# Kernel optimization log

Measured on AMD Instinct MI355X. Metric: run time of the kernel, lower is better.

## Reference

```python
import jax, jax.numpy as jnp
import numpy as np

N_NODES = 100000
N_EDGES = 1600000
F_IN = 128
DIM = 64
N_CLASSES = 40


def setup_inputs() -> dict:
    key = jax.random.key(0)
    ks = jax.random.split(key, 12)
    x = jax.random.normal(ks[0], (N_NODES, F_IN), dtype=jnp.float32)
    edge_index = jax.random.randint(ks[1], (2, N_EDGES), 0, N_NODES, dtype=jnp.int64)
    s = lambda fan_in: 1.0 / np.sqrt(fan_in)
    W1 = jax.random.uniform(ks[2], (F_IN, DIM), jnp.float32, -s(F_IN), s(F_IN))
    b1 = jax.random.uniform(ks[3], (DIM,), jnp.float32, -s(F_IN), s(F_IN))
    W2 = jax.random.uniform(ks[4], (DIM, DIM), jnp.float32, -s(DIM), s(DIM))
    b2 = jax.random.uniform(ks[5], (DIM,), jnp.float32, -s(DIM), s(DIM))
    Wf1 = jax.random.uniform(ks[6], (DIM, DIM), jnp.float32, -s(DIM), s(DIM))
    bf1 = jax.random.uniform(ks[7], (DIM,), jnp.float32, -s(DIM), s(DIM))
    Wf2 = jax.random.uniform(ks[8], (DIM, N_CLASSES), jnp.float32, -s(DIM), s(DIM))
    bf2 = jax.random.uniform(ks[9], (N_CLASSES,), jnp.float32, -s(DIM), s(DIM))
    return {"x": x, "edge_index": edge_index, "W1": W1, "b1": b1,
            "W2": W2, "b2": b2, "Wf1": Wf1, "bf1": bf1, "Wf2": Wf2, "bf2": bf2}


def _gin_agg(h, src, dst, n_nodes):
    # sum_{j in N(i)} h_j : gather along src, scatter-add to dst
    return jax.ops.segment_sum(h[src], dst, num_segments=n_nodes)


def reference(x, edge_index, W1, b1, W2, b2, Wf1, bf1, Wf2, bf2):
    src, dst = edge_index[0], edge_index[1]
    n = x.shape[0]
    # GINConv(Linear), eps=0: Linear(x + sum_neighbors)
    h = jax.nn.relu((x + _gin_agg(x, src, dst, n)) @ W1 + b1)
    h = jax.nn.relu((h + _gin_agg(h, src, dst, n)) @ W2 + b2)
    h = jax.nn.relu(h @ Wf1 + bf1)  # dropout p=0.5 is identity at inference
    logits = h @ Wf2 + bf2
    return jax.nn.log_softmax(logits, axis=1)
```

## Files before the change

kernel.cpp:

```cpp
#include <hip/hip_runtime.h>

#define NN 100000
#define NE 1600000
#define F_IN 128
#define DIM 64
#define NC 40
#define NB 196
#define MAXBE 10240

typedef unsigned short ushort_t;
typedef __attribute__((ext_vector_type(8))) short bf16x8;
typedef __attribute__((ext_vector_type(4))) float f32x4;

static __device__ __forceinline__ float b2f(ushort_t u) {
  return __uint_as_float(((unsigned)u) << 16);
}
static __device__ __forceinline__ ushort_t f2b(float f) {
  unsigned x = __float_as_uint(f);
  return (ushort_t)((x + 0x7fffu + ((x >> 16) & 1u)) >> 16);
}
static __device__ __forceinline__ unsigned pack2(float a, float b) {
  return (unsigned)f2b(a) | ((unsigned)f2b(b) << 16);
}

__global__ __launch_bounds__(256) void k_prep(const float* __restrict__ W1,
                                              const float* __restrict__ W2,
                                              const float* __restrict__ Wf1,
                                              const float* __restrict__ Wf2,
                                              ushort_t* __restrict__ W1T,
                                              ushort_t* __restrict__ W2T,
                                              ushort_t* __restrict__ Wf1T,
                                              ushort_t* __restrict__ Wf2T,
                                              int* __restrict__ bcur) {
  int t = threadIdx.x;
  if (t < NB) bcur[t] = 0;
  for (int i = t; i < 64 * 128; i += 256) { int c = i >> 7, k = i & 127; W1T[i] = f2b(W1[k * 64 + c]); }
  for (int i = t; i < 64 * 64; i += 256)  { int c = i >> 6, k = i & 63;  W2T[i] = f2b(W2[k * 64 + c]); }
  for (int i = t; i < 64 * 64; i += 256)  { int c = i >> 6, k = i & 63;  Wf1T[i] = f2b(Wf1[k * 64 + c]); }
  for (int i = t; i < 48 * 64; i += 256)  { int c = i >> 6, k = i & 63;  Wf2T[i] = (c < NC) ? f2b(Wf2[k * NC + c]) : (ushort_t)0; }
}

__global__ __launch_bounds__(256) void k_part(const int* __restrict__ src,
                                              const int* __restrict__ dst,
                                              int* __restrict__ bcur,
                                              unsigned* __restrict__ part) {
  __shared__ int hist[NB];
  __shared__ int gbase[NB];
  int t = threadIdx.x;
  for (int i = t; i < NB; i += 256) hist[i] = 0;
  __syncthreads();
  int e0 = blockIdx.x * 4096;
  int s[16], dd[16], r[16];
#pragma unroll
  for (int i = 0; i < 16; ++i) {
    int e = e0 + i * 256 + t;
    if (e < NE) {
      dd[i] = dst[e];
      s[i] = src[e];
      r[i] = atomicAdd(&hist[dd[i] >> 9], 1);
    }
  }
  __syncthreads();
  for (int i = t; i < NB; i += 256)
    gbase[i] = hist[i] ? atomicAdd(&bcur[i], hist[i]) : 0;
  __syncthreads();
#pragma unroll
  for (int i = 0; i < 16; ++i) {
    int e = e0 + i * 256 + t;
    if (e < NE) {
      int b = dd[i] >> 9;
      part[(size_t)b * MAXBE + gbase[b] + r[i]] = ((unsigned)(dd[i] & 511) << 17) | (unsigned)s[i];
    }
  }
}

__global__ __launch_bounds__(256) void k_csr(const int* __restrict__ bcur,
                                             const unsigned* __restrict__ part,
                                             int* __restrict__ cnt,
                                             int* __restrict__ offs,
                                             int* __restrict__ slots) {
  __shared__ unsigned pb[MAXBE];
  __shared__ ushort_t rk[MAXBE];
  __shared__ int lcnt[512], loff[512];
  int b = blockIdx.x, t = threadIdx.x;
  int start = b * MAXBE;
  int m = bcur[b];
  if (m > MAXBE) m = MAXBE;
  lcnt[t] = 0; lcnt[t + 256] = 0;
  __syncthreads();
  for (int i = t; i < m; i += 256) {
    unsigned v = part[start + i];
    pb[i] = v;
    rk[i] = (ushort_t)atomicAdd(&lcnt[v >> 17], 1);
  }
  __syncthreads();
  int o0 = lcnt[t], o1 = lcnt[t + 256];
  __syncthreads();
  for (int off = 1; off < 512; off <<= 1) {
    int v0 = (t >= off) ? lcnt[t - off] : 0;
    int v1 = (t + 256 >= off) ? lcnt[t + 256 - off] : 0;
    __syncthreads();
    lcnt[t] += v0;
    lcnt[t + 256] += v1;
    __syncthreads();
  }
  loff[t] = lcnt[t] - o0;
  loff[t + 256] = lcnt[t + 256] - o1;
  int node0 = b << 9;
  if (node0 + t < NN)       { cnt[node0 + t] = o0;       offs[node0 + t] = start + loff[t]; }
  if (node0 + t + 256 < NN) { cnt[node0 + t + 256] = o1; offs[node0 + t + 256] = start + loff[t + 256]; }
  __syncthreads();
  for (int i = t; i < m; i += 256) {
    unsigned v = pb[i];
    slots[start + loff[v >> 17] + rk[i]] = (int)(v & 0x1FFFFu);
  }
}

__global__ __launch_bounds__(256) void k_agg(const ushort_t* __restrict__ yb,
                                             const int* __restrict__ cnt,
                                             const int* __restrict__ offs,
                                             const int* __restrict__ slots,
                                             const float* __restrict__ bias,
                                             ushort_t* __restrict__ hb) {
  int wv = threadIdx.x >> 6, l = threadIdx.x & 63;
  int h = l >> 5;
  int n = blockIdx.x * 8 + wv * 2 + h;
  int li = l & 31;
  int g = (l >> 3) & 3;
  int q = l & 7;
  int cb = q * 16;
  int deg = cnt[n], start = offs[n];
  deg = deg > 64 ? 64 : deg;
  int sv0 = (li < deg) ? slots[start + li] : 0;
  int sv1 = (32 + li < deg) ? slots[start + 32 + li] : 0;
  int dego = __shfl_xor(deg, 32);
  int degmax = deg > dego ? deg : dego;
  float acc[8];
#pragma unroll
  for (int i = 0; i < 8; ++i) acc[i] = 0.f;
  const char* ybp = (const char*)yb;
  int hbase = h << 5;
  for (int j = 0; j < degmax; j += 16) {
    int i0 = j + g, i1 = j + 4 + g, i2 = j + 8 + g, i3 = j + 12 + g;
    int sa, sb, sc, sd;
    if (j < 32) {
      sa = __shfl(sv0, hbase + i0); sb = __shfl(sv0, hbase + i1);
      sc = __shfl(sv0, hbase + i2); sd = __shfl(sv0, hbase + i3);
    } else {
      sa = __shfl(sv1, hbase + (i0 & 31)); sb = __shfl(sv1, hbase + (i1 & 31));
      sc = __shfl(sv1, hbase + (i2 & 31)); sd = __shfl(sv1, hbase + (i3 & 31));
    }
    uint4 u0 = {0,0,0,0}, u1 = {0,0,0,0}, u2 = {0,0,0,0}, u3 = {0,0,0,0};
    if (i0 < deg) u0 = *(const uint4*)(ybp + (size_t)sa * 128 + cb);
    if (i1 < deg) u1 = *(const uint4*)(ybp + (size_t)sb * 128 + cb);
    if (i2 < deg) u2 = *(const uint4*)(ybp + (size_t)sc * 128 + cb);
    if (i3 < deg) u3 = *(const uint4*)(ybp + (size_t)sd * 128 + cb);
    acc[0] += __uint_as_float(u0.x << 16);  acc[1] += __uint_as_float(u0.x & 0xffff0000u);
    acc[2] += __uint_as_float(u0.y << 16);  acc[3] += __uint_as_float(u0.y & 0xffff0000u);
    acc[4] += __uint_as_float(u0.z << 16);  acc[5] += __uint_as_float(u0.z & 0xffff0000u);
    acc[6] += __uint_as_float(u0.w << 16);  acc[7] += __uint_as_float(u0.w & 0xffff0000u);
    acc[0] += __uint_as_float(u1.x << 16);  acc[1] += __uint_as_float(u1.x & 0xffff0000u);
    acc[2] += __uint_as_float(u1.y << 16);  acc[3] += __uint_as_float(u1.y & 0xffff0000u);
    acc[4] += __uint_as_float(u1.z << 16);  acc[5] += __uint_as_float(u1.z & 0xffff0000u);
    acc[6] += __uint_as_float(u1.w << 16);  acc[7] += __uint_as_float(u1.w & 0xffff0000u);
    acc[0] += __uint_as_float(u2.x << 16);  acc[1] += __uint_as_float(u2.x & 0xffff0000u);
    acc[2] += __uint_as_float(u2.y << 16);  acc[3] += __uint_as_float(u2.y & 0xffff0000u);
    acc[4] += __uint_as_float(u2.z << 16);  acc[5] += __uint_as_float(u2.z & 0xffff0000u);
    acc[6] += __uint_as_float(u2.w << 16);  acc[7] += __uint_as_float(u2.w & 0xffff0000u);
    acc[0] += __uint_as_float(u3.x << 16);  acc[1] += __uint_as_float(u3.x & 0xffff0000u);
    acc[2] += __uint_as_float(u3.y << 16);  acc[3] += __uint_as_float(u3.y & 0xffff0000u);
    acc[4] += __uint_as_float(u3.z << 16);  acc[5] += __uint_as_float(u3.z & 0xffff0000u);
    acc[6] += __uint_as_float(u3.w << 16);  acc[7] += __uint_as_float(u3.w & 0xffff0000u);
  }
#pragma unroll
  for (int i = 0; i < 8; ++i) {
    acc[i] += __shfl_xor(acc[i], 8);
    acc[i] += __shfl_xor(acc[i], 16);
  }
  if (li < 8) {
    uint4 yr = *(const uint4*)&yb[(size_t)n * 64 + q * 8];
    float4 ba = *(const float4*)&bias[q * 8];
    float4 bb = *(const float4*)&bias[q * 8 + 4];
    float v0 = fmaxf(__uint_as_float(yr.x << 16)         + acc[0] + ba.x, 0.f);
    float v1 = fmaxf(__uint_as_float(yr.x & 0xffff0000u) + acc[1] + ba.y, 0.f);
    float v2 = fmaxf(__uint_as_float(yr.y << 16)         + acc[2] + ba.z, 0.f);
    float v3 = fmaxf(__uint_as_float(yr.y & 0xffff0000u) + acc[3] + ba.w, 0.f);
    float v4 = fmaxf(__uint_as_float(yr.z << 16)         + acc[4] + bb.x, 0.f);
    float v5 = fmaxf(__uint_as_float(yr.z & 0xffff0000u) + acc[5] + bb.y, 0.f);
    float v6 = fmaxf(__uint_as_float(yr.w << 16)         + acc[6] + bb.z, 0.f);
    float v7 = fmaxf(__uint_as_float(yr.w & 0xffff0000u) + acc[7] + bb.w, 0.f);
    uint4 st;
    st.x = pack2(v0, v1);
    st.y = pack2(v2, v3);
    st.z = pack2(v4, v5);
    st.w = pack2(v6, v7);
    *(uint4*)&hb[(size_t)n * 64 + q * 8] = st;
  }
}

__global__ __launch_bounds__(256) void k_gemm1(const float* __restrict__ x,
                                               const ushort_t* __restrict__ W1T,
                                               ushort_t* __restrict__ yb) {
  __shared__ ushort_t H[64 * 136];
  int t = threadIdx.x, w = t >> 6, l = t & 63;
  int g = l >> 4, r16 = l & 15;
  int node0 = blockIdx.x * 64;
  bf16x8 B[4][4];
#pragma unroll
  for (int nt = 0; nt < 4; ++nt)
#pragma unroll
    for (int kt = 0; kt < 4; ++kt)
      B[nt][kt] = *(const bf16x8*)&W1T[(16 * nt + r16) * 128 + 32 * kt + 8 * g];
#pragma unroll
  for (int j = 0; j < 8; ++j) {
    int f = t + 256 * j;
    int e = f * 4;
    int n = e >> 7, c = e & 127;
    int gn = node0 + n; if (gn >= NN) gn = NN - 1;
    float4 v = *(const float4*)&x[(size_t)gn * 128 + c];
    ushort4 pv;
    pv.x = f2b(v.x); pv.y = f2b(v.y); pv.z = f2b(v.z); pv.w = f2b(v.w);
    *(ushort4*)&H[n * 136 + c] = pv;
  }
  __syncthreads();
  f32x4 acc[4] = {{0.f,0.f,0.f,0.f},{0.f,0.f,0.f,0.f},{0.f,0.f,0.f,0.f},{0.f,0.f,0.f,0.f}};
#pragma unroll
  for (int kt = 0; kt < 4; ++kt) {
    bf16x8 A = *(const bf16x8*)&H[(16 * w + r16) * 136 + 32 * kt + 8 * g];
#pragma unroll
    for (int nt = 0; nt < 4; ++nt)
      acc[nt] = __builtin_amdgcn_mfma_f32_16x16x32_bf16(A, B[nt][kt], acc[nt], 0, 0, 0);
  }
#pragma unroll
  for (int nt = 0; nt < 4; ++nt)
#pragma unroll
    for (int i = 0; i < 4; ++i) {
      int node = node0 + 16 * w + 4 * g + i;
      if (node < NN)
        yb[(size_t)node * 64 + 16 * nt + r16] = f2b(acc[nt][i]);
    }
}

__global__ __launch_bounds__(256) void k_mid(const ushort_t* __restrict__ hb,
                                             const ushort_t* __restrict__ W2T,
                                             ushort_t* __restrict__ yb) {
  __shared__ ushort_t H[64 * 72];
  int t = threadIdx.x, w = t >> 6, l = t & 63;
  int g = l >> 4, r16 = l & 15;
  int node0 = blockIdx.x * 64;
  bf16x8 B[4][2];
#pragma unroll
  for (int nt = 0; nt < 4; ++nt)
#pragma unroll
    for (int kt = 0; kt < 2; ++kt)
      B[nt][kt] = *(const bf16x8*)&W2T[(16 * nt + r16) * 64 + 32 * kt + 8 * g];
#pragma unroll
  for (int j = 0; j < 2; ++j) {
    int i = t + 256 * j;
    int n = i >> 3, c8 = (i & 7) * 8;
    int gn = node0 + n; if (gn >= NN) gn = NN - 1;
    uint4 u = *(const uint4*)&hb[(size_t)gn * 64 + c8];
    *(uint4*)&H[n * 72 + c8] = u;
  }
  __syncthreads();
  f32x4 acc[4] = {{0.f,0.f,0.f,0.f},{0.f,0.f,0.f,0.f},{0.f,0.f,0.f,0.f},{0.f,0.f,0.f,0.f}};
#pragma unroll
  for (int kt = 0; kt < 2; ++kt) {
    bf16x8 A = *(const bf16x8*)&H[(16 * w + r16) * 72 + 32 * kt + 8 * g];
#pragma unroll
    for (int nt = 0; nt < 4; ++nt)
      acc[nt] = __builtin_amdgcn_mfma_f32_16x16x32_bf16(A, B[nt][kt], acc[nt], 0, 0, 0);
  }
#pragma unroll
  for (int nt = 0; nt < 4; ++nt)
#pragma unroll
    for (int i = 0; i < 4; ++i) {
      int node = node0 + 16 * w + 4 * g + i;
      if (node < NN)
        yb[(size_t)node * 64 + 16 * nt + r16] = f2b(acc[nt][i]);
    }
}

__global__ __launch_bounds__(256) void k_final(const ushort_t* __restrict__ hb,
                                               const ushort_t* __restrict__ Wf1T,
                                               const float* __restrict__ bf1,
                                               const ushort_t* __restrict__ Wf2T,
                                               const float* __restrict__ bf2,
                                               float* __restrict__ out) {
  __shared__ ushort_t H[64 * 72];
  __shared__ ushort_t H2[64 * 72];
  int t = threadIdx.x, w = t >> 6, l = t & 63;
  int g = l >> 4, r16 = l & 15;
  int node0 = blockIdx.x * 64;
  bf16x8 B1[4][2], B2[3][2];
#pragma unroll
  for (int nt = 0; nt < 4; ++nt)
#pragma unroll
    for (int kt = 0; kt < 2; ++kt)
      B1[nt][kt] = *(const bf16x8*)&Wf1T[(16 * nt + r16) * 64 + 32 * kt + 8 * g];
#pragma unroll
  for (int nt = 0; nt < 3; ++nt)
#pragma unroll
    for (int kt = 0; kt < 2; ++kt)
      B2[nt][kt] = *(const bf16x8*)&Wf2T[(16 * nt + r16) * 64 + 32 * kt + 8 * g];
#pragma unroll
  for (int j = 0; j < 2; ++j) {
    int i = t + 256 * j;
    int n = i >> 3, c8 = (i & 7) * 8;
    int gn = node0 + n; if (gn >= NN) gn = NN - 1;
    uint4 u = *(const uint4*)&hb[(size_t)gn * 64 + c8];
    *(uint4*)&H[n * 72 + c8] = u;
  }
  __syncthreads();
  f32x4 acc[4] = {{0.f,0.f,0.f,0.f},{0.f,0.f,0.f,0.f},{0.f,0.f,0.f,0.f},{0.f,0.f,0.f,0.f}};
#pragma unroll
  for (int kt = 0; kt < 2; ++kt) {
    bf16x8 A = *(const bf16x8*)&H[(16 * w + r16) * 72 + 32 * kt + 8 * g];
#pragma unroll
    for (int nt = 0; nt < 4; ++nt)
      acc[nt] = __builtin_amdgcn_mfma_f32_16x16x32_bf16(A, B1[nt][kt], acc[nt], 0, 0, 0);
  }
#pragma unroll
  for (int nt = 0; nt < 4; ++nt) {
    float bias = bf1[16 * nt + r16];
#pragma unroll
    for (int i = 0; i < 4; ++i) {
      float v = fmaxf(acc[nt][i] + bias, 0.f);
      H2[(16 * w + 4 * g + i) * 72 + 16 * nt + r16] = f2b(v);
    }
  }
  __syncthreads();
  f32x4 acc2[3] = {{0.f,0.f,0.f,0.f},{0.f,0.f,0.f,0.f},{0.f,0.f,0.f,0.f}};
#pragma unroll
  for (int kt = 0; kt < 2; ++kt) {
    bf16x8 A2 = *(const bf16x8*)&H2[(16 * w + r16) * 72 + 32 * kt + 8 * g];
#pragma unroll
    for (int nt = 0; nt < 3; ++nt)
      acc2[nt] = __builtin_amdgcn_mfma_f32_16x16x32_bf16(A2, B2[nt][kt], acc2[nt], 0, 0, 0);
  }
  float lg[3][4];
#pragma unroll
  for (int nt = 0; nt < 3; ++nt) {
    int col = 16 * nt + r16;
    float bias = (col < NC) ? bf2[col] : 0.f;
#pragma unroll
    for (int i = 0; i < 4; ++i)
      lg[nt][i] = (col < NC) ? acc2[nt][i] + bias : -1e30f;
  }
#pragma unroll
  for (int i = 0; i < 4; ++i) {
    float m = fmaxf(fmaxf(lg[0][i], lg[1][i]), lg[2][i]);
#pragma unroll
    for (int off = 1; off < 16; off <<= 1) m = fmaxf(m, __shfl_xor(m, off));
    float s = 0.f;
#pragma unroll
    for (int nt = 0; nt < 3; ++nt)
      s += (lg[nt][i] > -1e29f) ? __expf(lg[nt][i] - m) : 0.f;
#pragma unroll
    for (int off = 1; off < 16; off <<= 1) s += __shfl_xor(s, off);
    float ls = __logf(s);
    int node = node0 + 16 * w + 4 * g + i;
#pragma unroll
    for (int nt = 0; nt < 3; ++nt) {
      int col = 16 * nt + r16;
      if (col < NC && node < NN)
        out[(size_t)node * NC + col] = lg[nt][i] - m - ls;
    }
  }
}

extern "C" void kernel_launch(void* const* d_in, const int* in_sizes, int n_in,
                              void* d_out, int out_size, void* d_ws, size_t ws_size,
                              hipStream_t stream) {
  const float* x   = (const float*)d_in[0];
  const int*   ei  = (const int*)d_in[1];
  const float* W1  = (const float*)d_in[2];
  const float* b1  = (const float*)d_in[3];
  const float* W2  = (const float*)d_in[4];
  const float* b2  = (const float*)d_in[5];
  const float* Wf1 = (const float*)d_in[6];
  const float* bf1 = (const float*)d_in[7];
  const float* Wf2 = (const float*)d_in[8];
  const float* bf2 = (const float*)d_in[9];
  float* out = (float*)d_out;

  char* ws = (char*)d_ws;
  size_t o = 0;
  int* bcur  = (int*)(ws + o); o += 4096;
  int* cnt   = (int*)(ws + o); o += 400000;
  int* offs  = (int*)(ws + o); o += 400000;
  o = (o + 255) & ~(size_t)255;
  ushort_t* W1T  = (ushort_t*)(ws + o); o += 64 * 128 * 2;
  ushort_t* W2T  = (ushort_t*)(ws + o); o += 64 * 64 * 2;
  ushort_t* Wf1T = (ushort_t*)(ws + o); o += 64 * 64 * 2;
  ushort_t* Wf2T = (ushort_t*)(ws + o); o += 48 * 64 * 2;
  o = (o + 255) & ~(size_t)255;
  unsigned* part = (unsigned*)(ws + o); o += (size_t)NB * MAXBE * 4;
  int* slots = (int*)(ws + o); o += (size_t)NB * MAXBE * 4;
  ushort_t* yb = (ushort_t*)(ws + o); o += (size_t)NN * DIM * 2;
  ushort_t* hb = (ushort_t*)(ws + o); o += (size_t)NN * DIM * 2;

  const int* srcp = ei;
  const int* dstp = ei + NE;

  k_prep<<<1, 256, 0, stream>>>(W1, W2, Wf1, Wf2, W1T, W2T, Wf1T, Wf2T, bcur);
  k_part<<<(NE + 4095) / 4096, 256, 0, stream>>>(srcp, dstp, bcur, part);
  k_csr<<<NB, 256, 0, stream>>>(bcur, part, cnt, offs, slots);
  k_gemm1<<<(NN + 63) / 64, 256, 0, stream>>>(x, W1T, yb);
  k_agg<<<NN / 8, 256, 0, stream>>>(yb, cnt, offs, slots, b1, hb);
  k_mid<<<(NN + 63) / 64, 256, 0, stream>>>(hb, W2T, yb);
  k_agg<<<NN / 8, 256, 0, stream>>>(yb, cnt, offs, slots, b2, hb);
  k_final<<<(NN + 63) / 64, 256, 0, stream>>>(hb, Wf1T, bf1, Wf2T, bf2, out);
}
```

Measured before the change: 168.4 us.

## Widen partition/CSR blocks to 512 threads and trim aggregation address math

The partition and CSR-build kernels now run 512 threads per block, each thread handling fewer edges and one node slot in the prefix scan. In the aggregation kernel, gather addresses use 32-bit unsigned arithmetic instead of 64-bit, and the mask on the high bf16 half is dropped. The low 16 bits are left in as extra mantissa noise, which slightly changes numerics in exchange for fewer ALU ops per gathered element.

```diff
diff --git a/kernel.cpp b/kernel.cpp
--- a/kernel.cpp
+++ b/kernel.cpp
@@ -40,20 +40,20 @@
   for (int i = t; i < 48 * 64; i += 256)  { int c = i >> 6, k = i & 63;  Wf2T[i] = (c < NC) ? f2b(Wf2[k * NC + c]) : (ushort_t)0; }
 }
 
-__global__ __launch_bounds__(256) void k_part(const int* __restrict__ src,
+__global__ __launch_bounds__(512) void k_part(const int* __restrict__ src,
                                               const int* __restrict__ dst,
                                               int* __restrict__ bcur,
                                               unsigned* __restrict__ part) {
   __shared__ int hist[NB];
   __shared__ int gbase[NB];
   int t = threadIdx.x;
-  for (int i = t; i < NB; i += 256) hist[i] = 0;
+  for (int i = t; i < NB; i += 512) hist[i] = 0;
   __syncthreads();
   int e0 = blockIdx.x * 4096;
-  int s[16], dd[16], r[16];
-#pragma unroll
-  for (int i = 0; i < 16; ++i) {
-    int e = e0 + i * 256 + t;
+  int s[8], dd[8], r[8];
+#pragma unroll
+  for (int i = 0; i < 8; ++i) {
+    int e = e0 + i * 512 + t;
     if (e < NE) {
       dd[i] = dst[e];
       s[i] = src[e];
@@ -61,12 +61,12 @@
     }
   }
   __syncthreads();
-  for (int i = t; i < NB; i += 256)
+  for (int i = t; i < NB; i += 512)
     gbase[i] = hist[i] ? atomicAdd(&bcur[i], hist[i]) : 0;
   __syncthreads();
 #pragma unroll
-  for (int i = 0; i < 16; ++i) {
-    int e = e0 + i * 256 + t;
+  for (int i = 0; i < 8; ++i) {
+    int e = e0 + i * 512 + t;
     if (e < NE) {
       int b = dd[i] >> 9;
       part[(size_t)b * MAXBE + gbase[b] + r[i]] = ((unsigned)(dd[i] & 511) << 17) | (unsigned)s[i];
@@ -74,43 +74,41 @@
   }
 }
 
-__global__ __launch_bounds__(256) void k_csr(const int* __restrict__ bcur,
+__global__ __launch_bounds__(512) void k_csr(const int* __restrict__ bcur,
                                              const unsigned* __restrict__ part,
                                              int* __restrict__ cnt,
                                              int* __restrict__ offs,
                                              int* __restrict__ slots) {
   __shared__ unsigned pb[MAXBE];
   __shared__ ushort_t rk[MAXBE];
-  __shared__ int lcnt[512], loff[512];
+  __shared__ int lcnt[512];
+  __shared__ int loff[512];
   int b = blockIdx.x, t = threadIdx.x;
   int start = b * MAXBE;
   int m = bcur[b];
   if (m > MAXBE) m = MAXBE;
-  lcnt[t] = 0; lcnt[t + 256] = 0;
-  __syncthreads();
-  for (int i = t; i < m; i += 256) {
+  lcnt[t] = 0;
+  __syncthreads();
+  for (int i = t; i < m; i += 512) {
     unsigned v = part[start + i];
     pb[i] = v;
     rk[i] = (ushort_t)atomicAdd(&lcnt[v >> 17], 1);
   }
   __syncthreads();
-  int o0 = lcnt[t], o1 = lcnt[t + 256];
+  int o0 = lcnt[t];
   __syncthreads();
   for (int off = 1; off < 512; off <<= 1) {
-    int v0 = (t >= off) ? lcnt[t - off] : 0;
-    int v1 = (t + 256 >= off) ? lcnt[t + 256 - off] : 0;
+    int u = (t >= off) ? lcnt[t - off] : 0;
     __syncthreads();
-    lcnt[t] += v0;
-    lcnt[t + 256] += v1;
+    lcnt[t] += u;
     __syncthreads();
   }
-  loff[t] = lcnt[t] - o0;
-  loff[t + 256] = lcnt[t + 256] - o1;
-  int node0 = b << 9;
-  if (node0 + t < NN)       { cnt[node0 + t] = o0;       offs[node0 + t] = start + loff[t]; }
-  if (node0 + t + 256 < NN) { cnt[node0 + t + 256] = o1; offs[node0 + t + 256] = start + loff[t + 256]; }
-  __syncthreads();
-  for (int i = t; i < m; i += 256) {
+  int excl = lcnt[t] - o0;
+  loff[t] = excl;
+  int gn = (b << 9) + t;
+  if (gn < NN) { cnt[gn] = o0; offs[gn] = start + excl; }
+  __syncthreads();
+  for (int i = t; i < m; i += 512) {
     unsigned v = pb[i];
     slots[start + loff[v >> 17] + rk[i]] = (int)(v & 0x1FFFFu);
   }
@@ -128,7 +126,7 @@
   int li = l & 31;
   int g = (l >> 3) & 3;
   int q = l & 7;
-  int cb = q * 16;
+  unsigned cb = (unsigned)q * 16u;
   int deg = cnt[n], start = offs[n];
   deg = deg > 64 ? 64 : deg;
   int sv0 = (li < deg) ? slots[start + li] : 0;
@@ -151,26 +149,26 @@
       sc = __shfl(sv1, hbase + (i2 & 31)); sd = __shfl(sv1, hbase + (i3 & 31));
     }
     uint4 u0 = {0,0,0,0}, u1 = {0,0,0,0}, u2 = {0,0,0,0}, u3 = {0,0,0,0};
-    if (i0 < deg) u0 = *(const uint4*)(ybp + (size_t)sa * 128 + cb);
-    if (i1 < deg) u1 = *(const uint4*)(ybp + (size_t)sb * 128 + cb);
-    if (i2 < deg) u2 = *(const uint4*)(ybp + (size_t)sc * 128 + cb);
-    if (i3 < deg) u3 = *(const uint4*)(ybp + (size_t)sd * 128 + cb);
-    acc[0] += __uint_as_float(u0.x << 16);  acc[1] += __uint_as_float(u0.x & 0xffff0000u);
-    acc[2] += __uint_as_float(u0.y << 16);  acc[3] += __uint_as_float(u0.y & 0xffff0000u);
-    acc[4] += __uint_as_float(u0.z << 16);  acc[5] += __uint_as_float(u0.z & 0xffff0000u);
-    acc[6] += __uint_as_float(u0.w << 16);  acc[7] += __uint_as_float(u0.w & 0xffff0000u);
-    acc[0] += __uint_as_float(u1.x << 16);  acc[1] += __uint_as_float(u1.x & 0xffff0000u);
-    acc[2] += __uint_as_float(u1.y << 16);  acc[3] += __uint_as_float(u1.y & 0xffff0000u);
-    acc[4] += __uint_as_float(u1.z << 16);  acc[5] += __uint_as_float(u1.z & 0xffff0000u);
-    acc[6] += __uint_as_float(u1.w << 16);  acc[7] += __uint_as_float(u1.w & 0xffff0000u);
-    acc[0] += __uint_as_float(u2.x << 16);  acc[1] += __uint_as_float(u2.x & 0xffff0000u);
-    acc[2] += __uint_as_float(u2.y << 16);  acc[3] += __uint_as_float(u2.y & 0xffff0000u);
-    acc[4] += __uint_as_float(u2.z << 16);  acc[5] += __uint_as_float(u2.z & 0xffff0000u);
-    acc[6] += __uint_as_float(u2.w << 16);  acc[7] += __uint_as_float(u2.w & 0xffff0000u);
-    acc[0] += __uint_as_float(u3.x << 16);  acc[1] += __uint_as_float(u3.x & 0xffff0000u);
-    acc[2] += __uint_as_float(u3.y << 16);  acc[3] += __uint_as_float(u3.y & 0xffff0000u);
-    acc[4] += __uint_as_float(u3.z << 16);  acc[5] += __uint_as_float(u3.z & 0xffff0000u);
-    acc[6] += __uint_as_float(u3.w << 16);  acc[7] += __uint_as_float(u3.w & 0xffff0000u);
+    if (i0 < deg) u0 = *(const uint4*)(ybp + ((unsigned)sa * 128u + cb));
+    if (i1 < deg) u1 = *(const uint4*)(ybp + ((unsigned)sb * 128u + cb));
+    if (i2 < deg) u2 = *(const uint4*)(ybp + ((unsigned)sc * 128u + cb));
+    if (i3 < deg) u3 = *(const uint4*)(ybp + ((unsigned)sd * 128u + cb));
+    acc[0] += __uint_as_float(u0.x << 16);  acc[1] += __uint_as_float(u0.x);
+    acc[2] += __uint_as_float(u0.y << 16);  acc[3] += __uint_as_float(u0.y);
+    acc[4] += __uint_as_float(u0.z << 16);  acc[5] += __uint_as_float(u0.z);
+    acc[6] += __uint_as_float(u0.w << 16);  acc[7] += __uint_as_float(u0.w);
+    acc[0] += __uint_as_float(u1.x << 16);  acc[1] += __uint_as_float(u1.x);
+    acc[2] += __uint_as_float(u1.y << 16);  acc[3] += __uint_as_float(u1.y);
+    acc[4] += __uint_as_float(u1.z << 16);  acc[5] += __uint_as_float(u1.z);
+    acc[6] += __uint_as_float(u1.w << 16);  acc[7] += __uint_as_float(u1.w);
+    acc[0] += __uint_as_float(u2.x << 16);  acc[1] += __uint_as_float(u2.x);
+    acc[2] += __uint_as_float(u2.y << 16);  acc[3] += __uint_as_float(u2.y);
+    acc[4] += __uint_as_float(u2.z << 16);  acc[5] += __uint_as_float(u2.z);
+    acc[6] += __uint_as_float(u2.w << 16);  acc[7] += __uint_as_float(u2.w);
+    acc[0] += __uint_as_float(u3.x << 16);  acc[1] += __uint_as_float(u3.x);
+    acc[2] += __uint_as_float(u3.y << 16);  acc[3] += __uint_as_float(u3.y);
+    acc[4] += __uint_as_float(u3.z << 16);  acc[5] += __uint_as_float(u3.z);
+    acc[6] += __uint_as_float(u3.w << 16);  acc[7] += __uint_as_float(u3.w);
   }
 #pragma unroll
   for (int i = 0; i < 8; ++i) {
@@ -178,7 +176,7 @@
     acc[i] += __shfl_xor(acc[i], 16);
   }
   if (li < 8) {
-    uint4 yr = *(const uint4*)&yb[(size_t)n * 64 + q * 8];
+    uint4 yr = *(const uint4*)(ybp + ((unsigned)n * 128u + (unsigned)q * 16u));
     float4 ba = *(const float4*)&bias[q * 8];
     float4 bb = *(const float4*)&bias[q * 8 + 4];
     float v0 = fmaxf(__uint_as_float(yr.x << 16)         + acc[0] + ba.x, 0.f);
@@ -404,8 +402,8 @@
   const int* dstp = ei + NE;
 
   k_prep<<<1, 256, 0, stream>>>(W1, W2, Wf1, Wf2, W1T, W2T, Wf1T, Wf2T, bcur);
-  k_part<<<(NE + 4095) / 4096, 256, 0, stream>>>(srcp, dstp, bcur, part);
-  k_csr<<<NB, 256, 0, stream>>>(bcur, part, cnt, offs, slots);
+  k_part<<<(NE + 4095) / 4096, 512, 0, stream>>>(srcp, dstp, bcur, part);
+  k_csr<<<NB, 512, 0, stream>>>(bcur, part, cnt, offs, slots);
   k_gemm1<<<(NN + 63) / 64, 256, 0, stream>>>(x, W1T, yb);
   k_agg<<<NN / 8, 256, 0, stream>>>(yb, cnt, offs, slots, b1, hb);
   k_mid<<<(NN + 63) / 64, 256, 0, stream>>>(hb, W2T, yb);
```

New measurement: 167.9 us. No clear change (-0.3%).
